# Kernel tuning notes

Measured on AMD Instinct MI355X. Metric: run time of the kernel, lower is better.

## Reference

```python
import jax, jax.numpy as jnp
import numpy as np
from jax import lax

EPS = 1e-06
B, C, T = 64, 80, 8000

def _inverse_sigmoid(v):
    v = min(1.0 - 1e-4, max(1e-4, float(v)))
    return float(np.log(v / (1.0 - v)))

def setup_inputs() -> dict:
    key = jax.random.key(0)
    features = jax.random.normal(key, (B, C, T), dtype=jnp.float32)
    logit_s = jnp.full((C,), _inverse_sigmoid(0.04), dtype=jnp.float32)
    alpha = jnp.full((C,), 0.96, dtype=jnp.float32)
    delta = jnp.full((C,), 2.0, dtype=jnp.float32)
    log_r = jnp.full((C,), np.log(0.5), dtype=jnp.float32)
    return {"features": features, "logit_s": logit_s, "alpha": alpha,
            "delta": delta, "log_r": log_r}

def reference(features, logit_s, alpha, delta, log_r):
    # features: [B, C, T]
    x = jnp.maximum(features, 0.0)
    s = jax.nn.sigmoid(logit_s)                      # [C]
    a = jnp.clip(alpha, 0.1, 1.0)[None, :, None]     # [1,C,1]
    d = jnp.maximum(delta, 0.1)[None, :, None]
    r = jnp.clip(jnp.exp(log_r), 0.05, 1.5)[None, :, None]
    # first-order IIR smoother m_t = (1-s)*m_{t-1} + s*x_t, m_0 = x_0
    xt = jnp.moveaxis(x, -1, 0)                      # [T, B, C]
    def step(prev, x_cur):
        cur = (1.0 - s) * prev + s * x_cur
        return cur, cur
    _, ms = lax.scan(step, xt[0], xt[1:])            # [T-1, B, C]
    m = jnp.concatenate([xt[:1], ms], axis=0)        # [T, B, C]
    m = jnp.moveaxis(m, 0, -1)                       # [B, C, T]
    pcen = jnp.power(x / jnp.power(EPS + m, a) + d, r) - jnp.power(d, r)
    return pcen
```

## Files before the change

### kernel.cpp

```cpp
#include <hip/hip_runtime.h>
#include <math.h>

#define PCEN_EPS 1e-6f

constexpr int Bn = 64, Cn = 80, Tn = 8000;
constexpr int ROWS = Bn * Cn;
constexpr int WPB  = 4;
constexpr int CHUNK = 256;
constexpr int NCHUNK = (Tn + CHUNK - 1) / CHUNK;

static_assert(ROWS % WPB == 0, "grid sizing");

__device__ __forceinline__ float fast_pow_pos(float b, float e) {
#if __has_builtin(__builtin_amdgcn_logf) && __has_builtin(__builtin_amdgcn_exp2f)
    return __builtin_amdgcn_exp2f(e * __builtin_amdgcn_logf(b));
#else
    return __exp2f(e * __log2f(b));
#endif
}

__global__ __launch_bounds__(WPB * 64, 4)
void pcen_kernel(const float* __restrict__ x,
                 const float* __restrict__ logit_s,
                 const float* __restrict__ alpha,
                 const float* __restrict__ delta,
                 const float* __restrict__ log_r,
                 float* __restrict__ out)
{
    const int lane = threadIdx.x & 63;
    const int wid  = threadIdx.x >> 6;
    const int row  = blockIdx.x * WPB + wid;
    const int c    = row % Cn;

    const float s  = 1.0f / (1.0f + __expf(-logit_s[c]));
    const float w  = 1.0f - s;
    const float a  = fminf(fmaxf(alpha[c], 0.1f), 1.0f);
    const float dd = fmaxf(delta[c], 0.1f);
    const float rr = fminf(fmaxf(__expf(log_r[c]), 0.05f), 1.5f);
    const float d_r = fast_pow_pos(dd, rr);
    const float na = -a;

    float w4p[6];
    w4p[0] = (w * w) * (w * w);
    #pragma unroll
    for (int i = 1; i < 6; ++i) w4p[i] = w4p[i - 1] * w4p[i - 1];
    float w4L = 1.0f;
    #pragma unroll
    for (int b = 0; b < 6; ++b)
        if (lane & (1 << b)) w4L *= w4p[b];

    const float* __restrict__ xrow = x + (size_t)row * Tn;
    float* __restrict__ orow       = out + (size_t)row * Tn;

    float P = fmaxf(xrow[0], 0.0f);

    int base = lane * 4;
    float4 xv = *reinterpret_cast<const float4*>(xrow + base);

    for (int ch = 0; ch < NCHUNK; ++ch) {
        float4 xn = make_float4(0.f, 0.f, 0.f, 0.f);
        const int nbase = base + CHUNK;
        if (ch + 1 < NCHUNK && nbase < Tn)
            xn = *reinterpret_cast<const float4*>(xrow + nbase);

        const float x0 = fmaxf(xv.x, 0.f), x1 = fmaxf(xv.y, 0.f);
        const float x2 = fmaxf(xv.z, 0.f), x3 = fmaxf(xv.w, 0.f);
        const float u0 = s * x0, u1 = s * x1, u2 = s * x2, u3 = s * x3;

        float y = fmaf(fmaf(fmaf(u0, w, u1), w, u2), w, u3);

        float Y = y;
        #pragma unroll
        for (int st = 0; st < 6; ++st) {
            const float Yup  = __shfl_up(Y, 1 << st, 64);
            const float cand = fmaf(w4p[st], Yup, Y);
            Y = (lane >= (1 << st)) ? cand : Y;
        }

        const float Yprev = __shfl_up(Y, 1, 64);
        const float excl  = (lane == 0) ? 0.0f : Yprev;
        const float F     = fmaf(w4L, P, excl);

        const float m0 = fmaf(w, F,  u0);
        const float m1 = fmaf(w, m0, u1);
        const float m2 = fmaf(w, m1, u2);
        const float m3 = fmaf(w, m2, u3);

        P = __shfl(m3, 63, 64);

        const float t0 = fast_pow_pos(PCEN_EPS + m0, na);
        const float t1 = fast_pow_pos(PCEN_EPS + m1, na);
        const float t2 = fast_pow_pos(PCEN_EPS + m2, na);
        const float t3 = fast_pow_pos(PCEN_EPS + m3, na);

        float4 ov;
        ov.x = fast_pow_pos(fmaf(x0, t0, dd), rr) - d_r;
        ov.y = fast_pow_pos(fmaf(x1, t1, dd), rr) - d_r;
        ov.z = fast_pow_pos(fmaf(x2, t2, dd), rr) - d_r;
        ov.w = fast_pow_pos(fmaf(x3, t3, dd), rr) - d_r;

        if (base < Tn)
            *reinterpret_cast<float4*>(orow + base) = ov;

        base += CHUNK;
        xv = xn;
    }
}

extern "C" void kernel_launch(void* const* d_in, const int* in_sizes, int n_in,
                              void* d_out, int out_size, void* d_ws, size_t ws_size,
                              hipStream_t stream) {
    const float* features = (const float*)d_in[0];
    const float* logit_s  = (const float*)d_in[1];
    const float* alpha    = (const float*)d_in[2];
    const float* delta    = (const float*)d_in[3];
    const float* log_r    = (const float*)d_in[4];
    float* out = (float*)d_out;

    const int blocks = ROWS / WPB;
    pcen_kernel<<<blocks, WPB * 64, 0, stream>>>(features, logit_s, alpha, delta, log_r, out);
}
```

Measured before the change: 70.57 us.

## Split each row across four waves with register-resident segments and cross-wave carry fixup

Each block now handles one row, and its four waves each scan a quarter of the time axis. Every wave loads its whole segment into registers up front, runs a per-chunk wave scan with 8 elements per lane, and then combines the segment carries through shared memory with a short serial fixup. It then adds the decayed incoming carry to each value before the pow computations. This removes the long serial 32-chunk dependency per wave, which should expose more memory parallelism, at the cost of higher register use and one block barrier.

```diff
diff --git a/kernel.cpp b/kernel.cpp
--- a/kernel.cpp
+++ b/kernel.cpp
@@ -5,11 +5,11 @@
 
 constexpr int Bn = 64, Cn = 80, Tn = 8000;
 constexpr int ROWS = Bn * Cn;
-constexpr int WPB  = 4;
-constexpr int CHUNK = 256;
-constexpr int NCHUNK = (Tn + CHUNK - 1) / CHUNK;
-
-static_assert(ROWS % WPB == 0, "grid sizing");
+constexpr int WPR  = 4;
+constexpr int SEG  = Tn / WPR;
+constexpr int EPL  = 8;
+constexpr int LCH  = 64 * EPL;
+constexpr int NCH  = (SEG + LCH - 1) / LCH;
 
 __device__ __forceinline__ float fast_pow_pos(float b, float e) {
 #if __has_builtin(__builtin_amdgcn_logf) && __has_builtin(__builtin_amdgcn_exp2f)
@@ -19,7 +19,7 @@
 #endif
 }
 
-__global__ __launch_bounds__(WPB * 64, 4)
+__global__ __launch_bounds__(256, 4)
 void pcen_kernel(const float* __restrict__ x,
                  const float* __restrict__ logit_s,
                  const float* __restrict__ alpha,
@@ -27,9 +27,10 @@
                  const float* __restrict__ log_r,
                  float* __restrict__ out)
 {
+    __shared__ float sm[WPR];
     const int lane = threadIdx.x & 63;
     const int wid  = threadIdx.x >> 6;
-    const int row  = blockIdx.x * WPB + wid;
+    const int row  = blockIdx.x;
     const int c    = row % Cn;
 
     const float s  = 1.0f / (1.0f + __expf(-logit_s[c]));
@@ -38,72 +39,94 @@
     const float dd = fmaxf(delta[c], 0.1f);
     const float rr = fminf(fmaxf(__expf(log_r[c]), 0.05f), 1.5f);
     const float d_r = fast_pow_pos(dd, rr);
-    const float na = -a;
+    const float na  = -a;
 
-    float w4p[6];
-    w4p[0] = (w * w) * (w * w);
-    #pragma unroll
-    for (int i = 1; i < 6; ++i) w4p[i] = w4p[i - 1] * w4p[i - 1];
-    float w4L = 1.0f;
+    float w8p[8];
+    {
+        const float w2 = w * w, w4 = w2 * w2;
+        w8p[0] = w4 * w4;
+        #pragma unroll
+        for (int i = 1; i < 8; ++i) w8p[i] = w8p[i - 1] * w8p[i - 1];
+    }
+    float w8L = 1.0f;
     #pragma unroll
     for (int b = 0; b < 6; ++b)
-        if (lane & (1 << b)) w4L *= w4p[b];
+        if (lane & (1 << b)) w8L *= w8p[b];
+    const float w512 = w8p[6];
+    const float w2000 = w8p[7] * w8p[6] * w8p[5] * w8p[4] * w8p[3] * w8p[1];
 
-    const float* __restrict__ xrow = x + (size_t)row * Tn;
-    float* __restrict__ orow       = out + (size_t)row * Tn;
+    const float* __restrict__ xs = x   + (size_t)row * Tn + wid * SEG;
+    float* __restrict__ os       = out + (size_t)row * Tn + wid * SEG;
 
-    float P = fmaxf(xrow[0], 0.0f);
+    float xv[NCH][EPL];
+    #pragma unroll
+    for (int ch = 0; ch < NCH; ++ch) {
+        const int base = ch * LCH + lane * EPL;
+        if (base + EPL <= SEG) {
+            const float4 p0 = *reinterpret_cast<const float4*>(xs + base);
+            const float4 p1 = *reinterpret_cast<const float4*>(xs + base + 4);
+            xv[ch][0] = p0.x; xv[ch][1] = p0.y; xv[ch][2] = p0.z; xv[ch][3] = p0.w;
+            xv[ch][4] = p1.x; xv[ch][5] = p1.y; xv[ch][6] = p1.z; xv[ch][7] = p1.w;
+        } else {
+            #pragma unroll
+            for (int j = 0; j < EPL; ++j) xv[ch][j] = 0.0f;
+        }
+    }
+    #pragma unroll
+    for (int ch = 0; ch < NCH; ++ch)
+        #pragma unroll
+        for (int j = 0; j < EPL; ++j) xv[ch][j] = fmaxf(xv[ch][j], 0.0f);
 
-    int base = lane * 4;
-    float4 xv = *reinterpret_cast<const float4*>(xrow + base);
+    float P = __shfl(xv[0][0], 0, 64);
+    if (wid != 0) P = 0.0f;
 
-    for (int ch = 0; ch < NCHUNK; ++ch) {
-        float4 xn = make_float4(0.f, 0.f, 0.f, 0.f);
-        const int nbase = base + CHUNK;
-        if (ch + 1 < NCHUNK && nbase < Tn)
-            xn = *reinterpret_cast<const float4*>(xrow + nbase);
-
-        const float x0 = fmaxf(xv.x, 0.f), x1 = fmaxf(xv.y, 0.f);
-        const float x2 = fmaxf(xv.z, 0.f), x3 = fmaxf(xv.w, 0.f);
-        const float u0 = s * x0, u1 = s * x1, u2 = s * x2, u3 = s * x3;
-
-        float y = fmaf(fmaf(fmaf(u0, w, u1), w, u2), w, u3);
-
+    float mv[NCH][EPL];
+    #pragma unroll
+    for (int ch = 0; ch < NCH; ++ch) {
+        float y = s * xv[ch][0];
+        #pragma unroll
+        for (int j = 1; j < EPL; ++j) y = fmaf(y, w, s * xv[ch][j]);
         float Y = y;
         #pragma unroll
         for (int st = 0; st < 6; ++st) {
             const float Yup  = __shfl_up(Y, 1 << st, 64);
-            const float cand = fmaf(w4p[st], Yup, Y);
+            const float cand = fmaf(w8p[st], Yup, Y);
             Y = (lane >= (1 << st)) ? cand : Y;
         }
-
         const float Yprev = __shfl_up(Y, 1, 64);
         const float excl  = (lane == 0) ? 0.0f : Yprev;
-        const float F     = fmaf(w4L, P, excl);
+        const float F     = fmaf(w8L, P, excl);
+        float mm = F;
+        #pragma unroll
+        for (int j = 0; j < EPL; ++j) { mm = fmaf(w, mm, s * xv[ch][j]); mv[ch][j] = mm; }
+        P = __shfl(mv[ch][EPL - 1], (ch == NCH - 1) ? 57 : 63, 64);
+    }
 
-        const float m0 = fmaf(w, F,  u0);
-        const float m1 = fmaf(w, m0, u1);
-        const float m2 = fmaf(w, m1, u2);
-        const float m3 = fmaf(w, m2, u3);
+    if (lane == 0) sm[wid] = P;
+    __syncthreads();
+    const float A0 = sm[0];
+    const float A1 = fmaf(w2000, A0, sm[1]);
+    const float A2 = fmaf(w2000, A1, sm[2]);
+    const float Pin = (wid == 1) ? A0 : (wid == 2) ? A1 : (wid == 3) ? A2 : 0.0f;
 
-        P = __shfl(m3, 63, 64);
-
-        const float t0 = fast_pow_pos(PCEN_EPS + m0, na);
-        const float t1 = fast_pow_pos(PCEN_EPS + m1, na);
-        const float t2 = fast_pow_pos(PCEN_EPS + m2, na);
-        const float t3 = fast_pow_pos(PCEN_EPS + m3, na);
-
-        float4 ov;
-        ov.x = fast_pow_pos(fmaf(x0, t0, dd), rr) - d_r;
-        ov.y = fast_pow_pos(fmaf(x1, t1, dd), rr) - d_r;
-        ov.z = fast_pow_pos(fmaf(x2, t2, dd), rr) - d_r;
-        ov.w = fast_pow_pos(fmaf(x3, t3, dd), rr) - d_r;
-
-        if (base < Tn)
-            *reinterpret_cast<float4*>(orow + base) = ov;
-
-        base += CHUNK;
-        xv = xn;
+    float wc = 1.0f;
+    #pragma unroll
+    for (int ch = 0; ch < NCH; ++ch) {
+        float f = wc * w8L * w;
+        float ov[EPL];
+        #pragma unroll
+        for (int j = 0; j < EPL; ++j) {
+            const float m = fmaf(f, Pin, mv[ch][j]);
+            f *= w;
+            const float t = fast_pow_pos(PCEN_EPS + m, na);
+            ov[j] = fast_pow_pos(fmaf(xv[ch][j], t, dd), rr) - d_r;
+        }
+        const int base = ch * LCH + lane * EPL;
+        if (base + EPL <= SEG) {
+            *reinterpret_cast<float4*>(os + base)     = make_float4(ov[0], ov[1], ov[2], ov[3]);
+            *reinterpret_cast<float4*>(os + base + 4) = make_float4(ov[4], ov[5], ov[6], ov[7]);
+        }
+        wc *= w512;
     }
 }
 
@@ -117,6 +140,5 @@
     const float* log_r    = (const float*)d_in[4];
     float* out = (float*)d_out;
 
-    const int blocks = ROWS / WPB;
-    pcen_kernel<<<blocks, WPB * 64, 0, stream>>>(features, logit_s, alpha, delta, log_r, out);
+    pcen_kernel<<<ROWS, WPR * 64, 0, stream>>>(features, logit_s, alpha, delta, log_r, out);
 }
```

New measurement: 63.88 us. -9.5%, faster.
